# Performance work log

Measured on AMD Instinct MI355X. Metric: run time of the kernel, lower is better.

The kernel has to match this reference:

```python
import jax, jax.numpy as jnp
import numpy as np

D = 768; NH = 12; HD = D // NH; L = 12; NC = 27; PATCH = 16; MLP = 3072; PROJ = 512
IMG = 224; GRID = IMG // PATCH; HW = GRID * GRID; S = NC + HW
NEG = -1e9

def _ln(x, w, b):
    m = jnp.mean(x, -1, keepdims=True)
    v = jnp.mean(jnp.square(x - m), -1, keepdims=True)
    return (x - m) * jax.lax.rsqrt(v + 1e-5) * w + b

def _quick_gelu(x):
    return x * jax.nn.sigmoid(1.702 * x)

def _build_mask(attn_obj_masks, dtype):
    # CRIS block mask: cls<->cls blocked except self; cls->patch allowed only for
    # patches of that class; patch->cls blocked; patch->patch fully allowed.
    B = attn_obj_masks.shape[0]
    oh = jax.nn.one_hot(attn_obj_masks, NC, dtype=dtype)              # [B, HW, NC]
    T11 = jnp.broadcast_to(1.0 - jnp.eye(NC, dtype=dtype), (B, NC, NC))
    M13 = 1.0 - jnp.swapaxes(oh, 1, 2)                                # [B, NC, HW]
    top = jnp.concatenate([T11, M13], axis=2)
    bot = jnp.concatenate([jnp.ones((B, HW, NC), dtype), jnp.zeros((B, HW, HW), dtype)], axis=2)
    Mb = jnp.concatenate([top, bot], axis=1)                          # [B, S, S]
    return jnp.where(Mb == 1.0, jnp.asarray(NEG, dtype), jnp.asarray(0.0, dtype))

def reference(img, sents, attn_obj_masks, obj_masks, cls_tokens, patch_w, patch_b, pos_embed,
              ln1_w, ln1_b, qkv_w, qkv_b, out_w, out_b, ln2_w, ln2_b,
              mlp_w1, mlp_b1, mlp_w2, mlp_b2, ln_post_w, ln_post_b, proj):
    B = img.shape[0]
    sents = sents / jnp.linalg.norm(sents, axis=-1, keepdims=True)    # encode_text output, L2 normed
    mask = _build_mask(attn_obj_masks, img.dtype)                     # [B, S, S]
    # patch embedding (conv stride 16) -> [B, HW, D]
    p = jax.lax.conv_general_dilated(img, patch_w, (PATCH, PATCH), 'VALID',
                                     dimension_numbers=('NCHW', 'OIHW', 'NCHW'))
    p = p.reshape(B, D, HW).transpose(0, 2, 1) + patch_b
    x = jnp.concatenate([jnp.broadcast_to(cls_tokens, (B, NC, D)), p], axis=1) + pos_embed
    scale = 1.0 / np.sqrt(HD).astype(np.float32)
    def block(x, prm):
        l1w, l1b, qw, qb, ow, ob, l2w, l2b, w1, b1, w2, b2 = prm
        h = _ln(x, l1w, l1b)
        qkv = h @ qw + qb
        q, k, v = jnp.split(qkv, 3, axis=-1)
        q = q.reshape(B, S, NH, HD).transpose(0, 2, 1, 3)
        k = k.reshape(B, S, NH, HD).transpose(0, 2, 1, 3)
        v = v.reshape(B, S, NH, HD).transpose(0, 2, 1, 3)
        scores = jnp.einsum('bhqd,bhkd->bhqk', q, k) * scale + mask[:, None]
        a = jax.nn.softmax(scores, axis=-1)
        o = jnp.einsum('bhqk,bhkd->bhqd', a, v).transpose(0, 2, 1, 3).reshape(B, S, D)
        x = x + o @ ow + ob
        h = _ln(x, l2w, l2b)
        x = x + _quick_gelu(h @ w1 + b1) @ w2 + b2
        return x, None
    x, _ = jax.lax.scan(block, x, (ln1_w, ln1_b, qkv_w, qkv_b, out_w, out_b,
                                   ln2_w, ln2_b, mlp_w1, mlp_b1, mlp_w2, mlp_b2))
    tokens = _ln(x, ln_post_w, ln_post_b) @ proj                      # [B, S, PROJ]
    obj = tokens[:, :NC]
    obj = obj / jnp.linalg.norm(obj, axis=-1, keepdims=True)
    pred_id = jnp.einsum('bnd,bd->bn', obj, sents)                    # [B, NC]
    # per-class scatter loop == gather of pred_id by per-pixel class id
    pred = jnp.take_along_axis(pred_id, obj_masks.reshape(B, -1), axis=1).reshape(obj_masks.shape)
    return pred                                                       # [B, 224, 224]

def setup_inputs():
    B = 16; std = 0.02
    ks = jax.random.split(jax.random.key(0), 16)
    f = jax.random.normal
    return {
        'img': f(ks[0], (B, 3, IMG, IMG), jnp.float32),
        'sents': f(ks[1], (B, PROJ), jnp.float32),
        'attn_obj_masks': jax.random.randint(ks[2], (B, HW), 0, NC, jnp.int32),
        'obj_masks': jax.random.randint(ks[3], (B, IMG, IMG), 0, NC, jnp.int32),
        'cls_tokens': f(ks[4], (1, NC, D)) * std,
        'patch_w': f(ks[5], (D, 3, PATCH, PATCH)) * std,
        'patch_b': jnp.zeros((D,)),
        'pos_embed': f(ks[6], (S, D)) * std,
        'ln1_w': jnp.ones((L, D)), 'ln1_b': jnp.zeros((L, D)),
        'qkv_w': f(ks[7], (L, D, 3 * D)) * std, 'qkv_b': jnp.zeros((L, 3 * D)),
        'out_w': f(ks[8], (L, D, D)) * std, 'out_b': jnp.zeros((L, D)),
        'ln2_w': jnp.ones((L, D)), 'ln2_b': jnp.zeros((L, D)),
        'mlp_w1': f(ks[9], (L, D, MLP)) * std, 'mlp_b1': jnp.zeros((L, MLP)),
        'mlp_w2': f(ks[10], (L, MLP, D)) * std, 'mlp_b2': jnp.zeros((L, D)),
        'ln_post_w': jnp.ones((D,)), 'ln_post_b': jnp.zeros((D,)),
        'proj': f(ks[11], (D, PROJ)) * std,
    }
```

## Files before the change

### kernel.cpp

```cpp
#include <hip/hip_runtime.h>

#define DEV __device__ __forceinline__

typedef short bf16x8 __attribute__((ext_vector_type(8)));
typedef float f32x4 __attribute__((ext_vector_type(4)));
typedef int vi4 __attribute__((ext_vector_type(4)));
typedef unsigned short u16;
typedef short short4v __attribute__((ext_vector_type(4)));

#define NEGV -1000000000.0f

DEV u16 f2bf(float f) {
  union { float f; unsigned u; } v; v.f = f;
  unsigned r = v.u + 0x7FFFu + ((v.u >> 16) & 1u);
  return (u16)(r >> 16);
}

DEV bf16x8 ld_bf8(const u16* p) {
  vi4 v = *(const vi4*)p;
  return __builtin_bit_cast(bf16x8, v);
}

DEV void gload_lds16(const u16* g, vi4* l) {
  __builtin_amdgcn_global_load_lds((const __attribute__((address_space(1))) void*)g,
                                   (__attribute__((address_space(3))) void*)l, 16, 0, 0);
}

template<int BN, int MODE, bool GELU, int KS>
__global__ __launch_bounds__(256) void gemm_bt(
    const u16* __restrict__ A, const u16* __restrict__ Bt,
    const float* __restrict__ bias,
    float* __restrict__ Cf, u16* __restrict__ Cb,
    int M, int N, int K, const float* __restrict__ pos)
{
  constexpr int FJ = BN / 32;
  constexpr int LB = BN / 64;
  constexpr int LTOT = 2 + LB;
  __shared__ vi4 As[2][512];
  __shared__ vi4 Bs[2][BN * 4];

  int gx = gridDim.x, gy = gridDim.y;
  int nwg = gx * gy * (int)gridDim.z;
  int orig = blockIdx.x + gx * (blockIdx.y + gy * blockIdx.z);
  int qq = nwg >> 3, rr = nwg & 7;
  int xcd = orig & 7, off = orig >> 3;
  int id = (xcd < rr) ? xcd * (qq + 1) + off : rr * (qq + 1) + (xcd - rr) * qq + off;
  int bx = id % gx, rest = id / gx, by = rest % gy, bz = rest / gy;

  int tid = threadIdx.x, lane = tid & 63, wid = tid >> 6;
  int wm = wid >> 1, wn = wid & 1;
  int m0 = by * 128, n0 = bx * BN;
  int kBeg = (K / KS) * bz, kEnd = kBeg + K / KS;
  f32x4 acc[4][FJ] = {};

  auto STAGE = [&](int buf, int kk) {
    #pragma unroll
    for (int r = 0; r < 2; ++r) {
      int flat = r * 256 + tid;
      int row = flat >> 2, c = flat & 3;
      int cs = c ^ ((row >> 1) & 3);
      gload_lds16(A + (long)(m0 + row) * K + kk + cs * 8, &As[buf][r * 256 + wid * 64]);
    }
    #pragma unroll
    for (int r = 0; r < LB; ++r) {
      int flat = r * 256 + tid;
      int row = flat >> 2, c = flat & 3;
      int cs = c ^ ((row >> 1) & 3);
      gload_lds16(Bt + (long)(n0 + row) * K + kk + cs * 8, &Bs[buf][r * 256 + wid * 64]);
    }
  };

  STAGE(0, kBeg);
  int cur = 0;
  for (int kk = kBeg; kk < kEnd; kk += 32) {
    if (kk + 32 < kEnd) {
      STAGE(cur ^ 1, kk + 32);
      asm volatile("s_waitcnt vmcnt(%0)" :: "i"(LTOT) : "memory");
    } else {
      asm volatile("s_waitcnt vmcnt(0)" ::: "memory");
    }
    __builtin_amdgcn_s_barrier();
    bf16x8 af[4], bfr[FJ];
    int cg = lane >> 4, l15 = lane & 15;
    #pragma unroll
    for (int i = 0; i < 4; ++i) {
      int ra = wm * 64 + i * 16 + l15;
      af[i] = __builtin_bit_cast(bf16x8, As[cur][ra * 4 + (cg ^ ((ra >> 1) & 3))]);
    }
    #pragma unroll
    for (int j = 0; j < FJ; ++j) {
      int rb = wn * (BN / 2) + j * 16 + l15;
      bfr[j] = __builtin_bit_cast(bf16x8, Bs[cur][rb * 4 + (cg ^ ((rb >> 1) & 3))]);
    }
    #pragma unroll
    for (int i = 0; i < 4; ++i)
      #pragma unroll
      for (int j = 0; j < FJ; ++j)
        acc[i][j] = __builtin_amdgcn_mfma_f32_16x16x32_bf16(af[i], bfr[j], acc[i][j], 0, 0, 0);
    __builtin_amdgcn_s_barrier();
    cur ^= 1;
  }

  int cg = lane >> 4, l15 = lane & 15;
  #pragma unroll
  for (int i = 0; i < 4; ++i) {
    #pragma unroll
    for (int j = 0; j < FJ; ++j) {
      int col = n0 + wn * (BN / 2) + j * 16 + l15;
      float bv = bias ? bias[col] : 0.f;
      #pragma unroll
      for (int r = 0; r < 4; ++r) {
        int row = m0 + wm * 64 + i * 16 + cg * 4 + r;
        if (row < M) {
          float v = acc[i][j][r];
          if (KS == 1 || bz == 0) v += bv;
          if (GELU) v = v / (1.f + __expf(-1.702f * v));
          if (MODE == 0) Cb[(long)row * N + col] = f2bf(v);
          else if (MODE == 1) {
            if (KS > 1) atomicAdd(&Cf[(long)row * N + col], v);
            else Cf[(long)row * N + col] += v;
          }
          else if (MODE == 2) Cf[(long)row * N + col] = v;
          else {
            int hw = row % 196;
            int xr = (row / 196) * 223 + 27 + hw;
            Cf[(long)xr * 768 + col] = v + pos[(27 + hw) * 768 + col];
          }
        }
      }
    }
  }
}

__global__ __launch_bounds__(256) void attn_kernel(
    const u16* __restrict__ QKV, const int* __restrict__ aom, u16* __restrict__ O)
{
  __shared__ vi4 Kl[224 * 8];
  __shared__ vi4 Vt[64 * 28];
  __shared__ vi4 Pl[4][16 * 28];
  __shared__ int ml[196];
  int tid = threadIdx.x, lane = tid & 63, wid = tid >> 6;
  int qg = blockIdx.x, h = blockIdx.y, b = blockIdx.z;
  long rowbase = (long)b * 223;
  #pragma unroll
  for (int it = 0; it < 7; ++it) {
    int flat = it * 256 + tid;
    int s = flat >> 3, c = flat & 7;
    int cs = c ^ (s & 7);
    gload_lds16(QKV + (rowbase + s) * 2304 + 768 + h * 64 + cs * 8, &Kl[it * 256 + wid * 64]);
  }
  u16* vt16 = (u16*)Vt;
  #pragma unroll
  for (int it = 0; it < 7; ++it) {
    int flat = it * 256 + tid;
    int s = flat >> 3, c = flat & 7;
    vi4 v = {0, 0, 0, 0};
    if (s < 223) v = *(const vi4*)(QKV + (rowbase + s) * 2304 + 1536 + h * 64 + c * 8);
    union { vi4 v4; u16 hx[8]; } uu; uu.v4 = v;
    int cs = s >> 3;
    #pragma unroll
    for (int j = 0; j < 8; ++j) {
      int d = c * 8 + j;
      vt16[d * 224 + (cs ^ ((d >> 1) & 3)) * 8 + (s & 7)] = uu.hx[j];
    }
  }
  for (int i = tid; i < 196; i += 256) ml[i] = aom[b * 196 + i];
  __syncthreads();

  int colk = lane & 15, cg = lane >> 4;
  #pragma unroll
  for (int rep = 0; rep < 2; ++rep) {
    int fo = wid * 2 + rep;
    if (fo >= 7) break;
    int qf = qg * 7 + fo;
    int q0 = qf * 16;
    int arow = q0 + colk; if (arow > 222) arow = 222;
    const u16* qb = QKV + (rowbase + arow) * 2304 + h * 64;
    bf16x8 aq0 = ld_bf8(qb + cg * 8);
    bf16x8 aq1 = ld_bf8(qb + 32 + cg * 8);

    f32x4 sc[14];
    #pragma unroll
    for (int kf = 0; kf < 14; ++kf) {
      int key = kf * 16 + colk;
      f32x4 a = {0.f, 0.f, 0.f, 0.f};
      bf16x8 bk0 = __builtin_bit_cast(bf16x8, Kl[key * 8 + (cg ^ (key & 7))]);
      bf16x8 bk1 = __builtin_bit_cast(bf16x8, Kl[key * 8 + ((4 + cg) ^ (key & 7))]);
      a = __builtin_amdgcn_mfma_f32_16x16x32_bf16(aq0, bk0, a, 0, 0, 0);
      a = __builtin_amdgcn_mfma_f32_16x16x32_bf16(aq1, bk1, a, 0, 0, 0);
      sc[kf] = a;
    }
    #pragma unroll
    for (int r = 0; r < 4; ++r) {
      int q = q0 + cg * 4 + r;
      float mx = -3.4e38f;
      #pragma unroll
      for (int kf = 0; kf < 14; ++kf) {
        int key = kf * 16 + colk;
        float mval;
        if (key >= 223) mval = NEGV;
        else if (q >= 27) mval = (key < 27) ? NEGV : 0.f;
        else if (key < 27) mval = (key == q) ? 0.f : NEGV;
        else mval = (ml[key - 27] == q) ? 0.f : NEGV;
        float s = sc[kf][r] * 0.125f + mval;
        sc[kf][r] = s;
        mx = fmaxf(mx, s);
      }
      #pragma unroll
      for (int d = 1; d < 16; d <<= 1) mx = fmaxf(mx, __shfl_xor(mx, d));
      float sum = 0.f;
      #pragma unroll
      for (int kf = 0; kf < 14; ++kf) {
        float e = __expf(sc[kf][r] - mx);
        sc[kf][r] = e; sum += e;
      }
      #pragma unroll
      for (int d = 1; d < 16; d <<= 1) sum += __shfl_xor(sum, d);
      float inv = 1.f / sum;
      #pragma unroll
      for (int kf = 0; kf < 14; ++kf) sc[kf][r] *= inv;
    }
    u16* pw = (u16*)Pl[wid];
    #pragma unroll
    for (int kf = 0; kf < 14; ++kf) {
      int key = kf * 16 + colk;
      int ck = key >> 3;
      #pragma unroll
      for (int r = 0; r < 4; ++r) {
        int prow = cg * 4 + r;
        pw[prow * 224 + (ck ^ ((prow >> 1) & 3)) * 8 + (key & 7)] = f2bf(sc[kf][r]);
      }
    }
    f32x4 oacc[4] = {};
    #pragma unroll
    for (int ks = 0; ks < 7; ++ks) {
      bf16x8 pa = __builtin_bit_cast(bf16x8, Pl[wid][colk * 28 + ((ks * 4 + cg) ^ ((colk >> 1) & 3))]);
      #pragma unroll
      for (int nf = 0; nf < 4; ++nf) {
        int d = nf * 16 + colk;
        bf16x8 bv = __builtin_bit_cast(bf16x8, Vt[d * 28 + ((ks * 4 + cg) ^ ((d >> 1) & 3))]);
        oacc[nf] = __builtin_amdgcn_mfma_f32_16x16x32_bf16(pa, bv, oacc[nf], 0, 0, 0);
      }
    }
    #pragma unroll
    for (int nf = 0; nf < 4; ++nf) {
      int d = h * 64 + nf * 16 + colk;
      #pragma unroll
      for (int r = 0; r < 4; ++r) {
        int q = q0 + cg * 4 + r;
        if (q < 223) O[(rowbase + q) * 768 + d] = f2bf(oacc[nf][r]);
      }
    }
  }
}

template<bool MAP27>
__global__ __launch_bounds__(256) void ln_kernel(
    const float* __restrict__ X, u16* __restrict__ Hb,
    const float* __restrict__ w, const float* __restrict__ bb, int nrows)
{
  int row = blockIdx.x * 4 + (threadIdx.x >> 6);
  if (row >= nrows) return;
  int xr = MAP27 ? (row / 27) * 223 + (row % 27) : row;
  int l = threadIdx.x & 63;
  const float4* xp = (const float4*)(X + (long)xr * 768);
  float4 a = xp[l], c = xp[l + 64], d = xp[l + 128];
  float s = a.x + a.y + a.z + a.w + c.x + c.y + c.z + c.w + d.x + d.y + d.z + d.w;
  #pragma unroll
  for (int t = 1; t < 64; t <<= 1) s += __shfl_xor(s, t);
  float mean = s * (1.f / 768.f);
  a.x -= mean; a.y -= mean; a.z -= mean; a.w -= mean;
  c.x -= mean; c.y -= mean; c.z -= mean; c.w -= mean;
  d.x -= mean; d.y -= mean; d.z -= mean; d.w -= mean;
  float q = a.x*a.x + a.y*a.y + a.z*a.z + a.w*a.w
          + c.x*c.x + c.y*c.y + c.z*c.z + c.w*c.w
          + d.x*d.x + d.y*d.y + d.z*d.z + d.w*d.w;
  #pragma unroll
  for (int t = 1; t < 64; t <<= 1) q += __shfl_xor(q, t);
  float rs = rsqrtf(q * (1.f / 768.f) + 1e-5f);
  const float4* wp = (const float4*)w;
  const float4* bp = (const float4*)bb;
  u16* out = Hb + (long)row * 768;
  float4 w0 = wp[l], w1 = wp[l + 64], w2 = wp[l + 128];
  float4 b0 = bp[l], b1 = bp[l + 64], b2 = bp[l + 128];
  short4v o;
  o[0] = (short)f2bf(a.x * rs * w0.x + b0.x); o[1] = (short)f2bf(a.y * rs * w0.y + b0.y);
  o[2] = (short)f2bf(a.z * rs * w0.z + b0.z); o[3] = (short)f2bf(a.w * rs * w0.w + b0.w);
  *(short4v*)(out + l * 4) = o;
  o[0] = (short)f2bf(c.x * rs * w1.x + b1.x); o[1] = (short)f2bf(c.y * rs * w1.y + b1.y);
  o[2] = (short)f2bf(c.z * rs * w1.z + b1.z); o[3] = (short)f2bf(c.w * rs * w1.w + b1.w);
  *(short4v*)(out + 256 + l * 4) = o;
  o[0] = (short)f2bf(d.x * rs * w2.x + b2.x); o[1] = (short)f2bf(d.y * rs * w2.y + b2.y);
  o[2] = (short)f2bf(d.z * rs * w2.z + b2.z); o[3] = (short)f2bf(d.w * rs * w2.w + b2.w);
  *(short4v*)(out + 512 + l * 4) = o;
}

__global__ __launch_bounds__(256) void transpose_w(
    const float* __restrict__ W, u16* __restrict__ WT, int K, int N, long sW, long sT)
{
  __shared__ float t[64][65];
  int z = blockIdx.z;
  W += (long)z * sW; WT += (long)z * sT;
  int n0 = blockIdx.x * 64, k0 = blockIdx.y * 64;
  #pragma unroll
  for (int i = 0; i < 4; ++i) {
    int flat = i * 256 + threadIdx.x;
    int r = flat >> 4, c = (flat & 15) * 4;
    float4 v = *(const float4*)(W + (long)(k0 + r) * N + n0 + c);
    t[r][c] = v.x; t[r][c + 1] = v.y; t[r][c + 2] = v.z; t[r][c + 3] = v.w;
  }
  __syncthreads();
  #pragma unroll
  for (int i = 0; i < 8; ++i) {
    int flat = i * 256 + threadIdx.x;
    int rn = flat >> 5, ck = (flat & 31) * 2;
    unsigned val = (unsigned)f2bf(t[ck][rn]) | ((unsigned)f2bf(t[ck + 1][rn]) << 16);
    *(unsigned*)(WT + (long)(n0 + rn) * K + k0 + ck) = val;
  }
}

__global__ void convert_bf16(const float* __restrict__ src, u16* __restrict__ dst, int n) {
  int i = blockIdx.x * 256 + threadIdx.x;
  if (i < n) dst[i] = f2bf(src[i]);
}

__global__ __launch_bounds__(256) void patch_extract(const float* __restrict__ img, u16* __restrict__ Xp) {
  int row = blockIdx.x;
  int b = row / 196, hw = row % 196, gh = hw / 14, gw = hw % 14;
  for (int idx = threadIdx.x; idx < 768; idx += 256) {
    int cch = idx >> 8, rem = idx & 255, kh = rem >> 4, kw = rem & 15;
    Xp[(long)row * 768 + idx] = f2bf(img[((long)(b * 3 + cch) * 224 + gh * 16 + kh) * 224 + gw * 16 + kw]);
  }
}

__global__ void cls_pos_fill(const float* __restrict__ cls, const float* __restrict__ pos, float* __restrict__ x) {
  int i = blockIdx.x * 256 + threadIdx.x;
  if (i >= 16 * 27 * 768) return;
  int d = i % 768, t = i / 768, b = t / 27, s = t % 27;
  x[((long)b * 223 + s) * 768 + d] = cls[s * 768 + d] + pos[s * 768 + d];
}

__global__ __launch_bounds__(256) void sents_norm(const float* __restrict__ s, float* __restrict__ sn) {
  __shared__ float sb[4];
  int b = blockIdx.x, t = threadIdx.x;
  float v0 = s[b * 512 + t], v1 = s[b * 512 + t + 256];
  float q = v0 * v0 + v1 * v1;
  #pragma unroll
  for (int d = 1; d < 64; d <<= 1) q += __shfl_xor(q, d);
  if ((t & 63) == 0) sb[t >> 6] = q;
  __syncthreads();
  float inv = rsqrtf(sb[0] + sb[1] + sb[2] + sb[3]);
  sn[b * 512 + t] = v0 * inv;
  sn[b * 512 + t + 256] = v1 * inv;
}

__global__ __launch_bounds__(256) void obj_dot(const float* __restrict__ obj, const float* __restrict__ sn, float* __restrict__ pid) {
  __shared__ float sb[8];
  int r = blockIdx.x, t = threadIdx.x, b = r / 27;
  float v0 = obj[(long)r * 512 + t], v1 = obj[(long)r * 512 + t + 256];
  float w0 = sn[b * 512 + t], w1 = sn[b * 512 + t + 256];
  float q = v0 * v0 + v1 * v1;
  float dt = v0 * w0 + v1 * w1;
  #pragma unroll
  for (int d = 1; d < 64; d <<= 1) { q += __shfl_xor(q, d); dt += __shfl_xor(dt, d); }
  if ((t & 63) == 0) { sb[t >> 6] = q; sb[4 + (t >> 6)] = dt; }
  __syncthreads();
  if (t == 0) pid[r] = (sb[4] + sb[5] + sb[6] + sb[7]) * rsqrtf(sb[0] + sb[1] + sb[2] + sb[3]);
}

__global__ void gather_pred(const int* __restrict__ om, const float* __restrict__ pid, float* __restrict__ out) {
  int i = blockIdx.x * 256 + threadIdx.x;
  if (i >= 16 * 224 * 224) return;
  int b = i / (224 * 224);
  out[i] = pid[b * 27 + om[i]];
}

extern "C" void kernel_launch(void* const* d_in, const int* in_sizes, int n_in,
                              void* d_out, int out_size, void* d_ws, size_t ws_size,
                              hipStream_t stream) {
  const float* img     = (const float*)d_in[0];
  const float* sents   = (const float*)d_in[1];
  const int*   aom     = (const int*)d_in[2];
  const int*   omask   = (const int*)d_in[3];
  const float* cls     = (const float*)d_in[4];
  const float* patch_w = (const float*)d_in[5];
  const float* patch_b = (const float*)d_in[6];
  const float* pos     = (const float*)d_in[7];
  const float* ln1w    = (const float*)d_in[8];
  const float* ln1b    = (const float*)d_in[9];
  const float* qkvw    = (const float*)d_in[10];
  const float* qkvb    = (const float*)d_in[11];
  const float* outw    = (const float*)d_in[12];
  const float* outb    = (const float*)d_in[13];
  const float* ln2w    = (const float*)d_in[14];
  const float* ln2b    = (const float*)d_in[15];
  const float* m1w     = (const float*)d_in[16];
  const float* m1b     = (const float*)d_in[17];
  const float* m2w     = (const float*)d_in[18];
  const float* m2b     = (const float*)d_in[19];
  const float* lnpw    = (const float*)d_in[20];
  const float* lnpb    = (const float*)d_in[21];
  const float* projw   = (const float*)d_in[22];

  char* p = (char*)d_ws;
  auto alloc = [&](size_t bytes) { char* r = p; p += (bytes + 255) & ~(size_t)255; return r; };
  float* x   = (float*)alloc(3568ul * 768 * 4);
  u16* H     = (u16*)alloc(3584ul * 768 * 2);
  u16* QKV   = (u16*)alloc(3584ul * 2304 * 2);
  u16* Obuf  = (u16*)alloc(3584ul * 768 * 2);
  u16* G     = (u16*)alloc(3584ul * 3072 * 2);
  u16* PWc   = (u16*)alloc(768ul * 768 * 2);
  u16* PrT   = (u16*)alloc(512ul * 768 * 2);
  float* obj = (float*)alloc(432ul * 512 * 4);
  float* sn  = (float*)alloc(16ul * 512 * 4);
  float* pid = (float*)alloc(432ul * 4);

  const size_t wlayer = (2304ul * 768 + 768ul * 768 + 3072ul * 768 + 768ul * 3072) * 2;
  size_t used = (size_t)(p - (char*)d_ws);
  int nw = (ws_size >= used + 12 * wlayer + 65536) ? 12 : 1;
  const long sQ = 2304l * 768, sO = 768l * 768, s1 = 768l * 3072, s2 = 3072l * 768;
  u16* WqT = (u16*)alloc((size_t)sQ * 2 * nw);
  u16* WoT = (u16*)alloc((size_t)sO * 2 * nw);
  u16* W1T = (u16*)alloc((size_t)s1 * 2 * nw);
  u16* W2T = (u16*)alloc((size_t)s2 * 2 * nw);

  convert_bf16<<<2304, 256, 0, stream>>>(patch_w, PWc, 768 * 768);
  transpose_w<<<dim3(8, 12, 1), 256, 0, stream>>>(projw, PrT, 768, 512, 0, 0);
  if (nw == 12) {
    transpose_w<<<dim3(36, 12, 12), 256, 0, stream>>>(qkvw, WqT, 768, 2304, sQ, sQ);
    transpose_w<<<dim3(12, 12, 12), 256, 0, stream>>>(outw, WoT, 768, 768, sO, sO);
    transpose_w<<<dim3(48, 12, 12), 256, 0, stream>>>(m1w, W1T, 768, 3072, s1, s1);
    transpose_w<<<dim3(12, 48, 12), 256, 0, stream>>>(m2w, W2T, 3072, 768, s2, s2);
  }
  patch_extract<<<3136, 256, 0, stream>>>(img, H);
  cls_pos_fill<<<1296, 256, 0, stream>>>(cls, pos, x);
  gemm_bt<64, 3, false, 1><<<dim3(12, 25), 256, 0, stream>>>(H, PWc, patch_b, x, nullptr, 3136, 768, 768, pos);

  for (int l = 0; l < 12; ++l) {
    u16 *wq, *wo, *w1, *w2;
    if (nw == 12) { wq = WqT + (long)l * sQ; wo = WoT + (long)l * sO; w1 = W1T + (long)l * s1; w2 = W2T + (long)l * s2; }
    else {
      wq = WqT; wo = WoT; w1 = W1T; w2 = W2T;
      transpose_w<<<dim3(36, 12, 1), 256, 0, stream>>>(qkvw + (long)l * sQ, wq, 768, 2304, 0, 0);
      transpose_w<<<dim3(12, 12, 1), 256, 0, stream>>>(outw + (long)l * sO, wo, 768, 768, 0, 0);
      transpose_w<<<dim3(48, 12, 1), 256, 0, stream>>>(m1w + (long)l * s1, w1, 768, 3072, 0, 0);
      transpose_w<<<dim3(12, 48, 1), 256, 0, stream>>>(m2w + (long)l * s2, w2, 3072, 768, 0, 0);
    }
    ln_kernel<false><<<892, 256, 0, stream>>>(x, H, ln1w + l * 768, ln1b + l * 768, 3568);
    gemm_bt<64, 0, false, 1><<<dim3(36, 28), 256, 0, stream>>>(H, wq, qkvb + l * 2304, nullptr, QKV, 3568, 2304, 768, nullptr);
    attn_kernel<<<dim3(2, 12, 16), 256, 0, stream>>>(QKV, aom, Obuf);
    gemm_bt<64, 1, false, 2><<<dim3(12, 28, 2), 256, 0, stream>>>(Obuf, wo, outb + l * 768, x, nullptr, 3568, 768, 768, nullptr);
    ln_kernel<false><<<892, 256, 0, stream>>>(x, H, ln2w + l * 768, ln2b + l * 768, 3568);
    gemm_bt<64, 0, true, 1><<<dim3(48, 28), 256, 0, stream>>>(H, w1, m1b + l * 3072, nullptr, G, 3568, 3072, 768, nullptr);
    gemm_bt<64, 1, false, 2><<<dim3(12, 28, 2), 256, 0, stream>>>(G, w2, m2b + l * 768, x, nullptr, 3568, 768, 3072, nullptr);
  }

  ln_kernel<true><<<108, 256, 0, stream>>>(x, H, lnpw, lnpb, 432);
  gemm_bt<64, 2, false, 1><<<dim3(8, 4), 256, 0, stream>>>(H, PrT, nullptr, obj, nullptr, 432, 512, 768, nullptr);
  sents_norm<<<16, 256, 0, stream>>>(sents, sn);
  obj_dot<<<432, 256, 0, stream>>>(obj, sn, pid);
  gather_pred<<<3136, 256, 0, stream>>>(omask, pid, (float*)d_out);
}
```

Before: 2.497 ms.

## Deepen GEMM K-tile to 64, widen QKV/MLP1 N-tile, vectorize patch extraction

The GEMM now stages a 64-wide K slice per buffer with an 8-chunk XOR swizzle. This halves the number of barriers and loop iterations per K. The QKV and MLP-up GEMMs switch to 128-wide N tiles, which raises reuse of the A tile but doubles LDS use and accumulator registers and halves the grid size. Patch extraction now uses float4 loads and short4 stores. The final projection becomes a split-K atomic GEMM with a preceding memset. Larger LDS and register footprints may lower occupancy.

```diff
diff --git a/kernel.cpp b/kernel.cpp
--- a/kernel.cpp
+++ b/kernel.cpp
@@ -34,10 +34,9 @@
     int M, int N, int K, const float* __restrict__ pos)
 {
   constexpr int FJ = BN / 32;
-  constexpr int LB = BN / 64;
-  constexpr int LTOT = 2 + LB;
-  __shared__ vi4 As[2][512];
-  __shared__ vi4 Bs[2][BN * 4];
+  constexpr int LTOT = 4 + FJ;
+  __shared__ vi4 As[2][1024];
+  __shared__ vi4 Bs[2][BN * 8];
 
   int gx = gridDim.x, gy = gridDim.y;
   int nwg = gx * gy * (int)gridDim.z;
@@ -50,53 +49,57 @@
   int tid = threadIdx.x, lane = tid & 63, wid = tid >> 6;
   int wm = wid >> 1, wn = wid & 1;
   int m0 = by * 128, n0 = bx * BN;
-  int kBeg = (K / KS) * bz, kEnd = kBeg + K / KS;
+  int kBeg = (K / KS) * bz;
+  int nT = (K / KS) >> 6;
   f32x4 acc[4][FJ] = {};
 
   auto STAGE = [&](int buf, int kk) {
     #pragma unroll
-    for (int r = 0; r < 2; ++r) {
+    for (int r = 0; r < 4; ++r) {
       int flat = r * 256 + tid;
-      int row = flat >> 2, c = flat & 3;
-      int cs = c ^ ((row >> 1) & 3);
+      int row = flat >> 3, c = flat & 7;
+      int cs = c ^ (row & 7);
       gload_lds16(A + (long)(m0 + row) * K + kk + cs * 8, &As[buf][r * 256 + wid * 64]);
     }
     #pragma unroll
-    for (int r = 0; r < LB; ++r) {
+    for (int r = 0; r < FJ; ++r) {
       int flat = r * 256 + tid;
-      int row = flat >> 2, c = flat & 3;
-      int cs = c ^ ((row >> 1) & 3);
+      int row = flat >> 3, c = flat & 7;
+      int cs = c ^ (row & 7);
       gload_lds16(Bt + (long)(n0 + row) * K + kk + cs * 8, &Bs[buf][r * 256 + wid * 64]);
     }
   };
 
   STAGE(0, kBeg);
   int cur = 0;
-  for (int kk = kBeg; kk < kEnd; kk += 32) {
-    if (kk + 32 < kEnd) {
-      STAGE(cur ^ 1, kk + 32);
+  for (int t = 0; t < nT; ++t) {
+    if (t + 1 < nT) {
+      STAGE(cur ^ 1, kBeg + (t + 1) * 64);
       asm volatile("s_waitcnt vmcnt(%0)" :: "i"(LTOT) : "memory");
     } else {
       asm volatile("s_waitcnt vmcnt(0)" ::: "memory");
     }
     __builtin_amdgcn_s_barrier();
-    bf16x8 af[4], bfr[FJ];
     int cg = lane >> 4, l15 = lane & 15;
     #pragma unroll
-    for (int i = 0; i < 4; ++i) {
-      int ra = wm * 64 + i * 16 + l15;
-      af[i] = __builtin_bit_cast(bf16x8, As[cur][ra * 4 + (cg ^ ((ra >> 1) & 3))]);
-    }
-    #pragma unroll
-    for (int j = 0; j < FJ; ++j) {
-      int rb = wn * (BN / 2) + j * 16 + l15;
-      bfr[j] = __builtin_bit_cast(bf16x8, Bs[cur][rb * 4 + (cg ^ ((rb >> 1) & 3))]);
-    }
-    #pragma unroll
-    for (int i = 0; i < 4; ++i)
-      #pragma unroll
-      for (int j = 0; j < FJ; ++j)
-        acc[i][j] = __builtin_amdgcn_mfma_f32_16x16x32_bf16(af[i], bfr[j], acc[i][j], 0, 0, 0);
+    for (int ks = 0; ks < 2; ++ks) {
+      bf16x8 af[4], bfr[FJ];
+      #pragma unroll
+      for (int i = 0; i < 4; ++i) {
+        int ra = wm * 64 + i * 16 + l15;
+        af[i] = __builtin_bit_cast(bf16x8, As[cur][ra * 8 + ((ks * 4 + cg) ^ (ra & 7))]);
+      }
+      #pragma unroll
+      for (int j = 0; j < FJ; ++j) {
+        int rb = wn * (BN / 2) + j * 16 + l15;
+        bfr[j] = __builtin_bit_cast(bf16x8, Bs[cur][rb * 8 + ((ks * 4 + cg) ^ (rb & 7))]);
+      }
+      #pragma unroll
+      for (int i = 0; i < 4; ++i)
+        #pragma unroll
+        for (int j = 0; j < FJ; ++j)
+          acc[i][j] = __builtin_amdgcn_mfma_f32_16x16x32_bf16(af[i], bfr[j], acc[i][j], 0, 0, 0);
+    }
     __builtin_amdgcn_s_barrier();
     cur ^= 1;
   }
@@ -324,13 +327,16 @@
   if (i < n) dst[i] = f2bf(src[i]);
 }
 
-__global__ __launch_bounds__(256) void patch_extract(const float* __restrict__ img, u16* __restrict__ Xp) {
+__global__ __launch_bounds__(192) void patch_extract(const float* __restrict__ img, u16* __restrict__ Xp) {
   int row = blockIdx.x;
+  int t = threadIdx.x;
+  int pair = t >> 2, part = t & 3;
+  int cch = pair >> 4, kh = pair & 15;
   int b = row / 196, hw = row % 196, gh = hw / 14, gw = hw % 14;
-  for (int idx = threadIdx.x; idx < 768; idx += 256) {
-    int cch = idx >> 8, rem = idx & 255, kh = rem >> 4, kw = rem & 15;
-    Xp[(long)row * 768 + idx] = f2bf(img[((long)(b * 3 + cch) * 224 + gh * 16 + kh) * 224 + gw * 16 + kw]);
-  }
+  float4 v = *(const float4*)(img + ((long)(b * 3 + cch) * 224 + gh * 16 + kh) * 224 + gw * 16 + part * 4);
+  short4v o;
+  o[0] = (short)f2bf(v.x); o[1] = (short)f2bf(v.y); o[2] = (short)f2bf(v.z); o[3] = (short)f2bf(v.w);
+  *(short4v*)(Xp + (long)row * 768 + pair * 16 + part * 4) = o;
 }
 
 __global__ void cls_pos_fill(const float* __restrict__ cls, const float* __restrict__ pos, float* __restrict__ x) {
@@ -432,7 +438,7 @@
     transpose_w<<<dim3(48, 12, 12), 256, 0, stream>>>(m1w, W1T, 768, 3072, s1, s1);
     transpose_w<<<dim3(12, 48, 12), 256, 0, stream>>>(m2w, W2T, 3072, 768, s2, s2);
   }
-  patch_extract<<<3136, 256, 0, stream>>>(img, H);
+  patch_extract<<<3136, 192, 0, stream>>>(img, H);
   cls_pos_fill<<<1296, 256, 0, stream>>>(cls, pos, x);
   gemm_bt<64, 3, false, 1><<<dim3(12, 25), 256, 0, stream>>>(H, PWc, patch_b, x, nullptr, 3136, 768, 768, pos);
 
@@ -447,16 +453,17 @@
       transpose_w<<<dim3(12, 48, 1), 256, 0, stream>>>(m2w + (long)l * s2, w2, 3072, 768, 0, 0);
     }
     ln_kernel<false><<<892, 256, 0, stream>>>(x, H, ln1w + l * 768, ln1b + l * 768, 3568);
-    gemm_bt<64, 0, false, 1><<<dim3(36, 28), 256, 0, stream>>>(H, wq, qkvb + l * 2304, nullptr, QKV, 3568, 2304, 768, nullptr);
+    gemm_bt<128, 0, false, 1><<<dim3(18, 28), 256, 0, stream>>>(H, wq, qkvb + l * 2304, nullptr, QKV, 3568, 2304, 768, nullptr);
     attn_kernel<<<dim3(2, 12, 16), 256, 0, stream>>>(QKV, aom, Obuf);
     gemm_bt<64, 1, false, 2><<<dim3(12, 28, 2), 256, 0, stream>>>(Obuf, wo, outb + l * 768, x, nullptr, 3568, 768, 768, nullptr);
     ln_kernel<false><<<892, 256, 0, stream>>>(x, H, ln2w + l * 768, ln2b + l * 768, 3568);
-    gemm_bt<64, 0, true, 1><<<dim3(48, 28), 256, 0, stream>>>(H, w1, m1b + l * 3072, nullptr, G, 3568, 3072, 768, nullptr);
+    gemm_bt<128, 0, true, 1><<<dim3(24, 28), 256, 0, stream>>>(H, w1, m1b + l * 3072, nullptr, G, 3568, 3072, 768, nullptr);
     gemm_bt<64, 1, false, 2><<<dim3(12, 28, 2), 256, 0, stream>>>(G, w2, m2b + l * 768, x, nullptr, 3568, 768, 3072, nullptr);
   }
 
   ln_kernel<true><<<108, 256, 0, stream>>>(x, H, lnpw, lnpb, 432);
-  gemm_bt<64, 2, false, 1><<<dim3(8, 4), 256, 0, stream>>>(H, PrT, nullptr, obj, nullptr, 432, 512, 768, nullptr);
+  hipMemsetAsync(obj, 0, 432ul * 512 * 4, stream);
+  gemm_bt<64, 1, false, 2><<<dim3(8, 4, 2), 256, 0, stream>>>(H, PrT, nullptr, obj, nullptr, 432, 512, 768, nullptr);
   sents_norm<<<16, 256, 0, stream>>>(sents, sn);
   obj_dot<<<432, 256, 0, stream>>>(obj, sn, pid);
   gather_pred<<<3136, 256, 0, stream>>>(omask, pid, (float*)d_out);
```

After: 2.479 ms. No clear change (-0.7%).
